# Kernel optimization log

Measured on AMD Instinct MI355X. Metric: run time of the kernel, lower is better.

## Reference

```python
import jax, jax.numpy as jnp
import numpy as np

B = 4096      # batch
D = 64        # state_dim
H = 512       # hidden_dim


def setup_inputs() -> dict:
    key = jax.random.key(0)
    ks = jax.random.split(key, 16)

    def init(k, shape, fan_in):
        return jax.random.normal(k, shape, dtype=jnp.float32) / np.float32(np.sqrt(fan_in))

    mu = jax.random.normal(ks[0], (B, D), dtype=jnp.float32)
    sigma_diag = 0.1 * jax.random.uniform(ks[1], (B, D), dtype=jnp.float32) + 0.01
    states = jnp.concatenate([mu, sigma_diag], axis=1)  # [B, 2D]

    return {
        "t": jnp.float32(0.5),
        "states": states,
        # dynamics net: tanh MLP D -> H -> H -> D
        "W1": init(ks[2], (H, D), D), "b1": jnp.zeros((H,), jnp.float32),
        "W2": init(ks[3], (H, H), H), "b2": jnp.zeros((H,), jnp.float32),
        "W3": init(ks[4], (D, H), H), "b3": jnp.zeros((D,), jnp.float32),
        # process-noise net: tanh MLP D -> H -> H -> D, softplus head (diagonal Q)
        "V1": init(ks[5], (H, D), D), "c1": jnp.zeros((H,), jnp.float32),
        "V2": init(ks[6], (H, H), H), "c2": jnp.zeros((H,), jnp.float32),
        "V3": init(ks[7], (D, H), H), "c3": jnp.zeros((D,), jnp.float32),
    }


def reference(t, states, W1, b1, W2, b2, W3, b3, V1, c1, V2, c2, V3, c3):
    # UPN ODE function, diagonal-covariance path.
    mu = states[:, :D]          # [B, D]
    sigma_diag = states[:, D:]  # [B, D]

    # dynamics MLP forward (t is an autonomous-system placeholder, unused)
    h1 = jnp.tanh(mu @ W1.T + b1)   # [B, H]
    h2 = jnp.tanh(h1 @ W2.T + b2)   # [B, H]
    mu_drift = h2 @ W3.T + b3       # [B, D]

    # analytic batched Jacobian of the tanh MLP: J = W3 diag(1-h2^2) W2 diag(1-h1^2) W1
    d1 = 1.0 - h1 * h1              # [B, H]
    d2 = 1.0 - h2 * h2              # [B, H]
    inner = jnp.einsum('hk,bk,kd->bhd', W2, d1, W1)   # [B, H, D]
    J = jnp.einsum('oh,bh,bhd->bod', W3, d2, inner)   # [B, D, D]
    J_diag = jnp.diagonal(J, axis1=1, axis2=2)        # [B, D]

    # process-noise net: diagonal Q, softplus ensures positivity
    g1 = jnp.tanh(mu @ V1.T + c1)
    g2 = jnp.tanh(g1 @ V2.T + c2)
    Q_diag = jax.nn.softplus(g2 @ V3.T + c3)          # [B, D]

    sigma_drift = 2.0 * J_diag * sigma_diag + Q_diag  # [B, D]
    return jnp.concatenate([mu_drift, sigma_drift], axis=1)  # [B, 2D]
```

## Files before the change

### kernel.cpp

```cpp
#include <hip/hip_runtime.h>
#include <hip/hip_bf16.h>

#define BB 4096
#define DD 64
#define HH 512

typedef __hip_bfloat16 bf16;
typedef _Float16 f16;
typedef __attribute__((ext_vector_type(8))) short bf16x8;
typedef __attribute__((ext_vector_type(8))) _Float16 f16x8;
typedef __attribute__((ext_vector_type(4))) float f32x4;

__device__ __forceinline__ float bf2f(bf16 x) { return __bfloat162float(x); }
__device__ __forceinline__ float u16tof(unsigned short u) {
  union { unsigned int i; float f; } v; v.i = ((unsigned int)u) << 16; return v.f;
}
#define BC8(p) __builtin_bit_cast(bf16x8, *(const uint4*)(p))
#define BCH8(p) __builtin_bit_cast(f16x8, *(const uint4*)(p))

__device__ __forceinline__ void gl16(const void* g, void* l) {
  __builtin_amdgcn_global_load_lds((__attribute__((address_space(1))) void*)g,
                                   (__attribute__((address_space(3))) void*)l,
                                   16, 0, 0);
}


__global__ __launch_bounds__(256) void cvt_weights(
    const float* __restrict__ W2, const float* __restrict__ V2,
    const float* __restrict__ W1, const float* __restrict__ V1,
    const float* __restrict__ W3, const float* __restrict__ V3,
    bf16* __restrict__ W2bf, bf16* __restrict__ V2bf,
    bf16* __restrict__ W1bf, bf16* __restrict__ V1bf,
    bf16* __restrict__ W3bf, bf16* __restrict__ V3bf,
    f16* __restrict__ W2fr, f16* __restrict__ W1sw, float* __restrict__ W3T) {
  int blk = blockIdx.x, t = threadIdx.x;
  if (blk < 512) {
    const float* src = (blk < 256) ? W2 : V2;
    bf16* dst = (blk < 256) ? W2bf : V2bf;
    int i = ((blk & 255) * 256 + t) * 4;
    float4 v = *(const float4*)(src + i);
    bf16 o[4] = {__float2bfloat16(v.x), __float2bfloat16(v.y),
                 __float2bfloat16(v.z), __float2bfloat16(v.w)};
    *(uint2*)(dst + i) = *(uint2*)o;
  } else if (blk < 640) {
    int uid = (blk - 512) * 256 + t;
    int col = (uid >> 2) & 511;
    int kc2s = uid >> 11;
    int kc = kc2s >> 1, s = kc2s & 1, q = uid & 3;
    const float* src = W2 + (size_t)col * HH + kc * 64 + s * 32 + q * 8;
    float4 a = *(const float4*)src;
    float4 b = *(const float4*)(src + 4);
    f16 o[8] = {(f16)a.x, (f16)a.y, (f16)a.z, (f16)a.w,
                (f16)b.x, (f16)b.y, (f16)b.z, (f16)b.w};
    *(uint4*)(W2fr + (size_t)uid * 8) = *(uint4*)o;
  } else if (blk < 656) {
    int uid = (blk - 640) * 256 + t;
    int kc = uid >> 9, rem = uid & 511;
    int dl = rem >> 3, u = rem & 7;
    f16 o[8];
#pragma unroll
    for (int e = 0; e < 8; ++e)
      o[e] = (f16)W1[(size_t)(kc * 64 + u * 8 + e) * DD + dl];
    *(uint4*)(W1sw + (size_t)((kc * 64 + dl) * 8 + (u ^ (dl & 7))) * 8) = *(uint4*)o;
  } else if (blk < 784) {
    int which = (blk - 656) >> 5;
    int local = (blk - 656) & 31;
    const float* src = (which == 0) ? W1 : (which == 1) ? V1 : (which == 2) ? W3 : V3;
    bf16* dst = (which == 0) ? W1bf : (which == 1) ? V1bf : (which == 2) ? W3bf : V3bf;
    int i = (local * 256 + t) * 4;
    float4 v = *(const float4*)(src + i);
    bf16 o[4] = {__float2bfloat16(v.x), __float2bfloat16(v.y),
                 __float2bfloat16(v.z), __float2bfloat16(v.w)};
    *(uint2*)(dst + i) = *(uint2*)o;
  } else {
    int e = ((blk - 784) * 256 + t) * 4;
    int h = e >> 6, o0 = e & 63;
    float o[4];
#pragma unroll
    for (int j = 0; j < 4; ++j) o[j] = W3[(size_t)(o0 + j) * HH + h];
    *(float4*)(W3T + (size_t)h * 64 + o0) = *(float4*)o;
  }
}

__global__ __launch_bounds__(256) void fwd(
    const float* __restrict__ states,
    const bf16* __restrict__ W1bf, const float* __restrict__ b1,
    const bf16* __restrict__ W2bf, const float* __restrict__ b2,
    const bf16* __restrict__ W3bf, const float* __restrict__ b3,
    const bf16* __restrict__ V1bf, const float* __restrict__ c1,
    const bf16* __restrict__ V2bf, const float* __restrict__ c2,
    const bf16* __restrict__ V3bf, const float* __restrict__ c3,
    bf16* __restrict__ Xbf, bf16* __restrict__ Ybf, float* __restrict__ out) {
  __shared__ __align__(16) bf16 mus[32 * 72];
  __shared__ __align__(16) bf16 Xres[32 * 520];
  __shared__ __align__(16) bf16 Bs[128 * 72];
  __shared__ __align__(16) bf16 Ych[32 * 136];
  const int bt = blockIdx.x * 32;
  const int path = blockIdx.y;
  const bf16* Wa = path ? V1bf : W1bf;
  const float* ba = path ? c1 : b1;
  const bf16* Wb = path ? V2bf : W2bf;
  const float* bbv = path ? c2 : b2;
  const bf16* Wc = path ? V3bf : W3bf;
  const float* bcv = path ? c3 : b3;
  const int t = threadIdx.x;
  const int lane = t & 63;
  const int w = t >> 6;
  const int c = lane & 15, q = lane >> 4;

  {
    int row = t >> 3, cg = (t & 7) * 8;
    bf16 o[8];
#pragma unroll
    for (int j = 0; j < 8; j += 4) {
      float4 v = *(const float4*)(states + (size_t)(bt + row) * 128 + cg + j);
      o[j] = __float2bfloat16(v.x); o[j + 1] = __float2bfloat16(v.y);
      o[j + 2] = __float2bfloat16(v.z); o[j + 3] = __float2bfloat16(v.w);
    }
    *(uint4*)(mus + row * 72 + cg) = *(const uint4*)o;
  }
  __syncthreads();

  for (int nch = 0; nch < 4; ++nch) {
    if (nch) __syncthreads();
#pragma unroll
    for (int i = 0; i < 4; ++i) {
      int g = t + i * 256;
      int row = g >> 3, kb = (g & 7) * 8;
      *(uint4*)(Bs + row * 72 + kb) =
          *(const uint4*)(Wa + (size_t)(nch * 128 + row) * 64 + kb);
    }
    __syncthreads();
    f32x4 acc1[2][2] = {};
#pragma unroll
    for (int s = 0; s < 2; ++s) {
      bf16x8 af0 = BC8(mus + c * 72 + s * 32 + q * 8);
      bf16x8 af1 = BC8(mus + (16 + c) * 72 + s * 32 + q * 8);
#pragma unroll
      for (int nt = 0; nt < 2; ++nt) {
        bf16x8 bfr = BC8(Bs + (w * 32 + nt * 16 + c) * 72 + s * 32 + q * 8);
        acc1[0][nt] = __builtin_amdgcn_mfma_f32_16x16x32_bf16(af0, bfr, acc1[0][nt], 0, 0, 0);
        acc1[1][nt] = __builtin_amdgcn_mfma_f32_16x16x32_bf16(af1, bfr, acc1[1][nt], 0, 0, 0);
      }
    }
#pragma unroll
    for (int nt = 0; nt < 2; ++nt) {
      int col = nch * 128 + w * 32 + nt * 16 + c;
      float bias = ba[col];
#pragma unroll
      for (int rb = 0; rb < 2; ++rb)
#pragma unroll
        for (int r = 0; r < 4; ++r) {
          int row = rb * 16 + q * 4 + r;
          float x = tanhf(acc1[rb][nt][r] + bias);
          Xres[row * 520 + col] = __float2bfloat16(x);
          if (!path) Xbf[(size_t)(bt + row) * HH + col] = __float2bfloat16(x);
        }
    }
  }
  __syncthreads();

  f32x4 acc3[2] = {};
  for (int hch = 0; hch < 4; ++hch) {
    f32x4 acc2[2][2] = {};
    for (int kc = 0; kc < 8; ++kc) {
      __syncthreads();
#pragma unroll
      for (int i = 0; i < 4; ++i) {
        int g = t + i * 256;
        int row = g >> 3, kb = (g & 7) * 8;
        *(uint4*)(Bs + row * 72 + kb) =
            *(const uint4*)(Wb + (size_t)(hch * 128 + row) * HH + kc * 64 + kb);
      }
      __syncthreads();
#pragma unroll
      for (int s = 0; s < 2; ++s) {
        bf16x8 af0 = BC8(Xres + c * 520 + kc * 64 + s * 32 + q * 8);
        bf16x8 af1 = BC8(Xres + (16 + c) * 520 + kc * 64 + s * 32 + q * 8);
#pragma unroll
        for (int nt = 0; nt < 2; ++nt) {
          bf16x8 bfr = BC8(Bs + (w * 32 + nt * 16 + c) * 72 + s * 32 + q * 8);
          acc2[0][nt] = __builtin_amdgcn_mfma_f32_16x16x32_bf16(af0, bfr, acc2[0][nt], 0, 0, 0);
          acc2[1][nt] = __builtin_amdgcn_mfma_f32_16x16x32_bf16(af1, bfr, acc2[1][nt], 0, 0, 0);
        }
      }
    }
    __syncthreads();
#pragma unroll
    for (int nt = 0; nt < 2; ++nt) {
      int hl = w * 32 + nt * 16 + c;
      int h = hch * 128 + hl;
      float bias = bbv[h];
#pragma unroll
      for (int rb = 0; rb < 2; ++rb)
#pragma unroll
        for (int r = 0; r < 4; ++r) {
          int row = rb * 16 + q * 4 + r;
          float y = tanhf(acc2[rb][nt][r] + bias);
          Ych[row * 136 + hl] = __float2bfloat16(y);
          if (!path) Ybf[(size_t)(bt + row) * HH + h] = __float2bfloat16(y);
        }
    }
    __syncthreads();
#pragma unroll
    for (int s3 = 0; s3 < 4; ++s3) {
      bf16x8 bf3 = BC8(Wc + (size_t)(w * 16 + c) * HH + hch * 128 + s3 * 32 + q * 8);
      bf16x8 af30 = BC8(Ych + c * 136 + s3 * 32 + q * 8);
      bf16x8 af31 = BC8(Ych + (16 + c) * 136 + s3 * 32 + q * 8);
      acc3[0] = __builtin_amdgcn_mfma_f32_16x16x32_bf16(af30, bf3, acc3[0], 0, 0, 0);
      acc3[1] = __builtin_amdgcn_mfma_f32_16x16x32_bf16(af31, bf3, acc3[1], 0, 0, 0);
    }
  }
  {
    int o = w * 16 + c;
    float bias = bcv[o];
#pragma unroll
    for (int rb = 0; rb < 2; ++rb)
#pragma unroll
      for (int r = 0; r < 4; ++r) {
        int row = rb * 16 + q * 4 + r;
        float v = acc3[rb][r] + bias;
        if (path) {
          v = fmaxf(v, 0.0f) + log1pf(expf(-fabsf(v)));
          out[(size_t)(bt + row) * 128 + 64 + o] = v;
        } else {
          out[(size_t)(bt + row) * 128 + o] = v;
        }
      }
  }
}

#define LDSW1 0
#define LDSD1 65536
#define LDSD2 73728
#define LDSRED 77824

__global__ __launch_bounds__(512, 2) void k4_gemm(
    const bf16* __restrict__ Xbf, const bf16* __restrict__ Ybf,
    const f16* __restrict__ W1sw, const f16* __restrict__ W2fr,
    const float* __restrict__ W3T, float* __restrict__ Jpart) {
  __shared__ __align__(16) char lds[81920];
  const int bt = blockIdx.x;
  const int h0 = blockIdx.y * 256;
  const int t = threadIdx.x;
  const int lane = t & 63;
  const int w = t >> 6;
  const int c = lane & 15, q = lane >> 4;
  const int wr = w >> 2, wc = w & 3;
  const int b0 = bt * 4;

#pragma unroll
  for (int i = 0; i < 8; ++i)
    gl16((const char*)W1sw + (t + i * 512) * 16,
         (char*)lds + LDSW1 + (t + i * 512) * 16);
  {
    int e = t * 4, j = e >> 9, k = e & 511;
    ushort4 xv = *(const ushort4*)((const unsigned short*)Xbf +
                                   (size_t)(b0 + j) * HH + k);
    f16 o[4];
    float x;
    x = u16tof(xv.x); o[0] = (f16)(1.f - x * x);
    x = u16tof(xv.y); o[1] = (f16)(1.f - x * x);
    x = u16tof(xv.z); o[2] = (f16)(1.f - x * x);
    x = u16tof(xv.w); o[3] = (f16)(1.f - x * x);
    *(uint2*)(lds + LDSD1 + e * 2) = *(uint2*)o;
  }
  {
    int e = t * 2, j = e >> 8, n = e & 255;
    ushort2 yv = *(const ushort2*)((const unsigned short*)Ybf +
                                   (size_t)(b0 + j) * HH + h0 + n);
    float y0 = u16tof(yv.x), y1 = u16tof(yv.y);
    float2 d2v = {1.f - y0 * y0, 1.f - y1 * y1};
    *(float2*)(lds + LDSD2 + e * 4) = d2v;
  }
  __syncthreads();

  const int cj = c & 7;
  const int j16_0 = ((0 + q) ^ cj) * 16;
  const int j16_1 = ((4 + q) ^ cj) * 16;
  const int arow = c * 128;
  const char* d1b = (const char*)lds + LDSD1 + wr * 2048 + q * 16;

  const char* gB = (const char*)W2fr + (size_t)(h0 + wc * 64) * 64 +
                   (c * 64 + q * 16);
#define BLD(kc_, s_, nt_) \
  BCH8(gB + ((kc_) * 2 + (s_)) * 32768 + (nt_) * 1024)

  f16x8 bb0[2][4], bb1[2][4];
#pragma unroll
  for (int nt = 0; nt < 4; ++nt) bb0[0][nt] = BLD(0, 0, nt);
#pragma unroll
  for (int nt = 0; nt < 4; ++nt) bb1[0][nt] = BLD(0, 1, nt);

  f32x4 acc[8][4] = {};

#pragma unroll
  for (int kc = 0; kc < 8; ++kc) {
    const int cur = kc & 1, nxt = cur ^ 1;
    if (kc < 7) {
#pragma unroll
      for (int nt = 0; nt < 4; ++nt) bb0[nxt][nt] = BLD(kc + 1, 0, nt);
#pragma unroll
      for (int nt = 0; nt < 4; ++nt) bb1[nxt][nt] = BLD(kc + 1, 1, nt);
    }
    const char* Ab = (const char*)lds + LDSW1 + kc * 8192;
    f16x8 a0[4], a1[4];
#pragma unroll
    for (int i = 0; i < 4; ++i) a0[i] = BCH8(Ab + arow + i * 2048 + j16_0);
#pragma unroll
    for (int i = 0; i < 4; ++i) a1[i] = BCH8(Ab + arow + i * 2048 + j16_1);
    f16x8 d00 = BCH8(d1b + kc * 128);
    f16x8 d10 = BCH8(d1b + 1024 + kc * 128);
    f16x8 d01 = BCH8(d1b + 64 + kc * 128);
    f16x8 d11 = BCH8(d1b + 1024 + 64 + kc * 128);

    f16x8 av;
    __builtin_amdgcn_s_setprio(1);
#pragma unroll
    for (int mt = 0; mt < 4; ++mt) {
      av = a0[mt] * d00;
#pragma unroll
      for (int nt = 0; nt < 4; ++nt)
        acc[mt][nt] = __builtin_amdgcn_mfma_f32_16x16x32_f16(
            av, bb0[cur][nt], acc[mt][nt], 0, 0, 0);
    }
#pragma unroll
    for (int mt = 0; mt < 4; ++mt) {
      av = a0[mt] * d10;
#pragma unroll
      for (int nt = 0; nt < 4; ++nt)
        acc[mt + 4][nt] = __builtin_amdgcn_mfma_f32_16x16x32_f16(
            av, bb0[cur][nt], acc[mt + 4][nt], 0, 0, 0);
    }
#pragma unroll
    for (int mt = 0; mt < 4; ++mt) {
      av = a1[mt] * d01;
#pragma unroll
      for (int nt = 0; nt < 4; ++nt)
        acc[mt][nt] = __builtin_amdgcn_mfma_f32_16x16x32_f16(
            av, bb1[cur][nt], acc[mt][nt], 0, 0, 0);
    }
#pragma unroll
    for (int mt = 0; mt < 4; ++mt) {
      av = a1[mt] * d11;
#pragma unroll
      for (int nt = 0; nt < 4; ++nt)
        acc[mt + 4][nt] = __builtin_amdgcn_mfma_f32_16x16x32_f16(
            av, bb1[cur][nt], acc[mt + 4][nt], 0, 0, 0);
    }
    __builtin_amdgcn_s_setprio(0);
    __builtin_amdgcn_sched_barrier(0);
  }
  __syncthreads();

#pragma unroll
  for (int i = 0; i < 8; ++i) {
    int e = (t + i * 512) * 4;
    int col = e >> 6, dl0 = e & 63;
    float4 v = *(const float4*)(W3T + (size_t)(h0 + col) * 64 + dl0);
    *(float4*)(lds + (col * 72 + dl0) * 4) = v;
  }
  __syncthreads();

  float d2r[2][4];
#pragma unroll
  for (int bh = 0; bh < 2; ++bh)
#pragma unroll
    for (int nt = 0; nt < 4; ++nt)
      d2r[bh][nt] = *(const float*)(
          lds + LDSD2 + ((wr * 2 + bh) * 256 + wc * 64 + nt * 16 + c) * 4);

  float vsum[8][4] = {};
#pragma unroll
  for (int mt4 = 0; mt4 < 4; ++mt4)
#pragma unroll
    for (int nt = 0; nt < 4; ++nt) {
      f32x4 w3v = *(const f32x4*)(
          lds + ((wc * 64 + nt * 16 + c) * 72 + mt4 * 16 + q * 4) * 4);
#pragma unroll
      for (int bh = 0; bh < 2; ++bh) {
        const int mt = bh * 4 + mt4;
        float sc = d2r[bh][nt];
#pragma unroll
        for (int r = 0; r < 4; ++r)
          vsum[mt][r] += acc[mt][nt][r] * w3v[r] * sc;
      }
    }

#pragma unroll
  for (int mt = 0; mt < 8; ++mt)
#pragma unroll
    for (int r = 0; r < 4; ++r) {
      float v = vsum[mt][r];
      v += __shfl_xor(v, 1);
      v += __shfl_xor(v, 2);
      v += __shfl_xor(v, 4);
      v += __shfl_xor(v, 8);
      if (c == 0)
        *(float*)(lds + LDSRED +
                  (wc * 256 + wr * 128 + mt * 16 + q * 4 + r) * 4) = v;
    }
  __syncthreads();
  if (t < 256) {
    float J = *(const float*)(lds + LDSRED + t * 4) +
              *(const float*)(lds + LDSRED + (256 + t) * 4) +
              *(const float*)(lds + LDSRED + (512 + t) * 4) +
              *(const float*)(lds + LDSRED + (768 + t) * 4);
    Jpart[(size_t)blockIdx.y * (BB * 64) + (size_t)bt * 256 + t] = J;
  }
}

__global__ __launch_bounds__(256) void combine(
    const float* __restrict__ Jpart, const float* __restrict__ states,
    float* __restrict__ out) {
  int idx = blockIdx.x * 256 + threadIdx.x;
  int b = idx >> 6, d = idx & 63;
  const int plane = BB * 64;
  float J = Jpart[idx] + Jpart[plane + idx];
  float sig = states[(size_t)b * 128 + 64 + d];
  float qd = out[(size_t)b * 128 + 64 + d];
  out[(size_t)b * 128 + 64 + d] = 2.0f * J * sig + qd;
}

extern "C" void kernel_launch(void* const* d_in, const int* in_sizes, int n_in,
                              void* d_out, int out_size, void* d_ws, size_t ws_size,
                              hipStream_t stream) {
  const float* states = (const float*)d_in[1];
  const float* W1 = (const float*)d_in[2];
  const float* b1 = (const float*)d_in[3];
  const float* W2 = (const float*)d_in[4];
  const float* b2 = (const float*)d_in[5];
  const float* W3 = (const float*)d_in[6];
  const float* b3 = (const float*)d_in[7];
  const float* V1 = (const float*)d_in[8];
  const float* c1 = (const float*)d_in[9];
  const float* V2 = (const float*)d_in[10];
  const float* c2 = (const float*)d_in[11];
  const float* V3 = (const float*)d_in[12];
  const float* c3 = (const float*)d_in[13];
  float* out = (float*)d_out;

  bf16* Xbf = (bf16*)d_ws;
  bf16* Ybf = Xbf + (size_t)BB * HH;
  bf16* W2bf = Ybf + (size_t)BB * HH;
  bf16* V2bf = W2bf + (size_t)HH * HH;
  bf16* W1bf = V2bf + (size_t)HH * HH;
  bf16* V1bf = W1bf + (size_t)HH * DD;
  bf16* W3bf = V1bf + (size_t)HH * DD;
  bf16* V3bf = W3bf + (size_t)DD * HH;
  f16* W1sw = (f16*)(V3bf + (size_t)DD * HH);
  f16* W2fr = W1sw + (size_t)DD * HH;
  float* W3T = (float*)(W2fr + (size_t)HH * HH);
  float* Jpart = W3T + (size_t)HH * DD;

  cvt_weights<<<dim3(816), 256, 0, stream>>>(W2, V2, W1, V1, W3, V3,
                                             W2bf, V2bf, W1bf, V1bf,
                                             W3bf, V3bf, W2fr, W1sw, W3T);
  fwd<<<dim3(128, 2), 256, 0, stream>>>(states, W1bf, b1, W2bf, b2, W3bf, b3,
                                        V1bf, c1, V2bf, c2, V3bf, c3,
                                        Xbf, Ybf, out);
  k4_gemm<<<dim3(1024, 2), 512, 0, stream>>>(Xbf, Ybf, W1sw, W2fr, W3T, Jpart);
  combine<<<dim3(1024), 256, 0, stream>>>(Jpart, states, out);
}
```

Before: 275.9 us.

## Make Jacobian kernel persistent over batch tiles and fuse combine step

The Jacobian GEMM kernel becomes a persistent grid of 256 blocks, each looping over four batch tiles and both hidden halves. The swizzled W1 tile is loaded into LDS once per block instead of once per tile, and the separate combine kernel and Jpart buffer are removed by accumulating the two halves in LDS and writing the sigma drift directly. W3T is now read from global memory instead of being staged in LDS, and the s_setprio hints are dropped. The risks are lower parallelism with 256 blocks of 512 threads, and a possible LDS race: the next tile writes new d1/d2 values before any barrier separates it from the previous tile's final reads.

```diff
diff --git a/kernel.cpp b/kernel.cpp
--- a/kernel.cpp
+++ b/kernel.cpp
@@ -234,192 +234,183 @@
 #define LDSD1 65536
 #define LDSD2 73728
 #define LDSRED 77824
+#define LDSJ 81920
 
 __global__ __launch_bounds__(512, 2) void k4_gemm(
     const bf16* __restrict__ Xbf, const bf16* __restrict__ Ybf,
     const f16* __restrict__ W1sw, const f16* __restrict__ W2fr,
-    const float* __restrict__ W3T, float* __restrict__ Jpart) {
-  __shared__ __align__(16) char lds[81920];
-  const int bt = blockIdx.x;
-  const int h0 = blockIdx.y * 256;
+    const float* __restrict__ W3T, const float* __restrict__ states,
+    float* __restrict__ out) {
+  __shared__ __align__(16) char lds[82944];
+  const int cu = blockIdx.x;
   const int t = threadIdx.x;
   const int lane = t & 63;
   const int w = t >> 6;
   const int c = lane & 15, q = lane >> 4;
   const int wr = w >> 2, wc = w & 3;
-  const int b0 = bt * 4;
-
-#pragma unroll
-  for (int i = 0; i < 8; ++i)
-    gl16((const char*)W1sw + (t + i * 512) * 16,
-         (char*)lds + LDSW1 + (t + i * 512) * 16);
-  {
-    int e = t * 4, j = e >> 9, k = e & 511;
-    ushort4 xv = *(const ushort4*)((const unsigned short*)Xbf +
-                                   (size_t)(b0 + j) * HH + k);
-    f16 o[4];
-    float x;
-    x = u16tof(xv.x); o[0] = (f16)(1.f - x * x);
-    x = u16tof(xv.y); o[1] = (f16)(1.f - x * x);
-    x = u16tof(xv.z); o[2] = (f16)(1.f - x * x);
-    x = u16tof(xv.w); o[3] = (f16)(1.f - x * x);
-    *(uint2*)(lds + LDSD1 + e * 2) = *(uint2*)o;
-  }
-  {
-    int e = t * 2, j = e >> 8, n = e & 255;
-    ushort2 yv = *(const ushort2*)((const unsigned short*)Ybf +
-                                   (size_t)(b0 + j) * HH + h0 + n);
-    float y0 = u16tof(yv.x), y1 = u16tof(yv.y);
-    float2 d2v = {1.f - y0 * y0, 1.f - y1 * y1};
-    *(float2*)(lds + LDSD2 + e * 4) = d2v;
-  }
-  __syncthreads();
-
   const int cj = c & 7;
   const int j16_0 = ((0 + q) ^ cj) * 16;
   const int j16_1 = ((4 + q) ^ cj) * 16;
   const int arow = c * 128;
   const char* d1b = (const char*)lds + LDSD1 + wr * 2048 + q * 16;
 
-  const char* gB = (const char*)W2fr + (size_t)(h0 + wc * 64) * 64 +
-                   (c * 64 + q * 16);
+#pragma unroll
+  for (int i = 0; i < 8; ++i)
+    gl16((const char*)W1sw + (t + i * 512) * 16,
+         (char*)lds + LDSW1 + (t + i * 512) * 16);
+
+#pragma unroll 1
+  for (int jt = 0; jt < 8; ++jt) {
+    const int bt = cu + (jt >> 1) * 256;
+    const int y = jt & 1;
+    const int h0 = y * 256;
+    const int b0 = bt * 4;
+
+    if (y == 0) {
+      int e = t * 4, j = e >> 9, k = e & 511;
+      ushort4 xv = *(const ushort4*)((const unsigned short*)Xbf +
+                                     (size_t)(b0 + j) * HH + k);
+      f16 o[4];
+      float x;
+      x = u16tof(xv.x); o[0] = (f16)(1.f - x * x);
+      x = u16tof(xv.y); o[1] = (f16)(1.f - x * x);
+      x = u16tof(xv.z); o[2] = (f16)(1.f - x * x);
+      x = u16tof(xv.w); o[3] = (f16)(1.f - x * x);
+      *(uint2*)(lds + LDSD1 + e * 2) = *(uint2*)o;
+    }
+    {
+      int e = t * 2, j = e >> 8, n = e & 255;
+      ushort2 yv = *(const ushort2*)((const unsigned short*)Ybf +
+                                     (size_t)(b0 + j) * HH + h0 + n);
+      float y0 = u16tof(yv.x), y1 = u16tof(yv.y);
+      float2 d2v = {1.f - y0 * y0, 1.f - y1 * y1};
+      *(float2*)(lds + LDSD2 + e * 4) = d2v;
+    }
+    __syncthreads();
+
+    const char* gB = (const char*)W2fr + (size_t)(h0 + wc * 64) * 64 +
+                     (c * 64 + q * 16);
 #define BLD(kc_, s_, nt_) \
   BCH8(gB + ((kc_) * 2 + (s_)) * 32768 + (nt_) * 1024)
 
-  f16x8 bb0[2][4], bb1[2][4];
-#pragma unroll
-  for (int nt = 0; nt < 4; ++nt) bb0[0][nt] = BLD(0, 0, nt);
-#pragma unroll
-  for (int nt = 0; nt < 4; ++nt) bb1[0][nt] = BLD(0, 1, nt);
-
-  f32x4 acc[8][4] = {};
-
-#pragma unroll
-  for (int kc = 0; kc < 8; ++kc) {
-    const int cur = kc & 1, nxt = cur ^ 1;
-    if (kc < 7) {
-#pragma unroll
-      for (int nt = 0; nt < 4; ++nt) bb0[nxt][nt] = BLD(kc + 1, 0, nt);
-#pragma unroll
-      for (int nt = 0; nt < 4; ++nt) bb1[nxt][nt] = BLD(kc + 1, 1, nt);
-    }
-    const char* Ab = (const char*)lds + LDSW1 + kc * 8192;
-    f16x8 a0[4], a1[4];
-#pragma unroll
-    for (int i = 0; i < 4; ++i) a0[i] = BCH8(Ab + arow + i * 2048 + j16_0);
-#pragma unroll
-    for (int i = 0; i < 4; ++i) a1[i] = BCH8(Ab + arow + i * 2048 + j16_1);
-    f16x8 d00 = BCH8(d1b + kc * 128);
-    f16x8 d10 = BCH8(d1b + 1024 + kc * 128);
-    f16x8 d01 = BCH8(d1b + 64 + kc * 128);
-    f16x8 d11 = BCH8(d1b + 1024 + 64 + kc * 128);
-
-    f16x8 av;
-    __builtin_amdgcn_s_setprio(1);
-#pragma unroll
-    for (int mt = 0; mt < 4; ++mt) {
-      av = a0[mt] * d00;
+    f16x8 bb0[2][4], bb1[2][4];
+#pragma unroll
+    for (int nt = 0; nt < 4; ++nt) bb0[0][nt] = BLD(0, 0, nt);
+#pragma unroll
+    for (int nt = 0; nt < 4; ++nt) bb1[0][nt] = BLD(0, 1, nt);
+
+    f32x4 acc[8][4] = {};
+
+#pragma unroll
+    for (int kc = 0; kc < 8; ++kc) {
+      const int cur = kc & 1, nxt = cur ^ 1;
+      if (kc < 7) {
+#pragma unroll
+        for (int nt = 0; nt < 4; ++nt) bb0[nxt][nt] = BLD(kc + 1, 0, nt);
+#pragma unroll
+        for (int nt = 0; nt < 4; ++nt) bb1[nxt][nt] = BLD(kc + 1, 1, nt);
+      }
+      const char* Ab = (const char*)lds + LDSW1 + kc * 8192;
+      f16x8 a0[4], a1[4];
+#pragma unroll
+      for (int i = 0; i < 4; ++i) a0[i] = BCH8(Ab + arow + i * 2048 + j16_0);
+#pragma unroll
+      for (int i = 0; i < 4; ++i) a1[i] = BCH8(Ab + arow + i * 2048 + j16_1);
+      f16x8 d00 = BCH8(d1b + kc * 128);
+      f16x8 d10 = BCH8(d1b + 1024 + kc * 128);
+      f16x8 d01 = BCH8(d1b + 64 + kc * 128);
+      f16x8 d11 = BCH8(d1b + 1024 + 64 + kc * 128);
+
+      f16x8 av;
+#pragma unroll
+      for (int mt = 0; mt < 4; ++mt) {
+        av = a0[mt] * d00;
+#pragma unroll
+        for (int nt = 0; nt < 4; ++nt)
+          acc[mt][nt] = __builtin_amdgcn_mfma_f32_16x16x32_f16(
+              av, bb0[cur][nt], acc[mt][nt], 0, 0, 0);
+      }
+#pragma unroll
+      for (int mt = 0; mt < 4; ++mt) {
+        av = a0[mt] * d10;
+#pragma unroll
+        for (int nt = 0; nt < 4; ++nt)
+          acc[mt + 4][nt] = __builtin_amdgcn_mfma_f32_16x16x32_f16(
+              av, bb0[cur][nt], acc[mt + 4][nt], 0, 0, 0);
+      }
+#pragma unroll
+      for (int mt = 0; mt < 4; ++mt) {
+        av = a1[mt] * d01;
+#pragma unroll
+        for (int nt = 0; nt < 4; ++nt)
+          acc[mt][nt] = __builtin_amdgcn_mfma_f32_16x16x32_f16(
+              av, bb1[cur][nt], acc[mt][nt], 0, 0, 0);
+      }
+#pragma unroll
+      for (int mt = 0; mt < 4; ++mt) {
+        av = a1[mt] * d11;
+#pragma unroll
+        for (int nt = 0; nt < 4; ++nt)
+          acc[mt + 4][nt] = __builtin_amdgcn_mfma_f32_16x16x32_f16(
+              av, bb1[cur][nt], acc[mt + 4][nt], 0, 0, 0);
+      }
+      __builtin_amdgcn_sched_barrier(0);
+    }
+
+    float d2r[2][4];
+#pragma unroll
+    for (int bh = 0; bh < 2; ++bh)
 #pragma unroll
       for (int nt = 0; nt < 4; ++nt)
-        acc[mt][nt] = __builtin_amdgcn_mfma_f32_16x16x32_f16(
-            av, bb0[cur][nt], acc[mt][nt], 0, 0, 0);
-    }
-#pragma unroll
-    for (int mt = 0; mt < 4; ++mt) {
-      av = a0[mt] * d10;
-#pragma unroll
-      for (int nt = 0; nt < 4; ++nt)
-        acc[mt + 4][nt] = __builtin_amdgcn_mfma_f32_16x16x32_f16(
-            av, bb0[cur][nt], acc[mt + 4][nt], 0, 0, 0);
-    }
-#pragma unroll
-    for (int mt = 0; mt < 4; ++mt) {
-      av = a1[mt] * d01;
-#pragma unroll
-      for (int nt = 0; nt < 4; ++nt)
-        acc[mt][nt] = __builtin_amdgcn_mfma_f32_16x16x32_f16(
-            av, bb1[cur][nt], acc[mt][nt], 0, 0, 0);
-    }
-#pragma unroll
-    for (int mt = 0; mt < 4; ++mt) {
-      av = a1[mt] * d11;
-#pragma unroll
-      for (int nt = 0; nt < 4; ++nt)
-        acc[mt + 4][nt] = __builtin_amdgcn_mfma_f32_16x16x32_f16(
-            av, bb1[cur][nt], acc[mt + 4][nt], 0, 0, 0);
-    }
-    __builtin_amdgcn_s_setprio(0);
-    __builtin_amdgcn_sched_barrier(0);
-  }
-  __syncthreads();
-
-#pragma unroll
-  for (int i = 0; i < 8; ++i) {
-    int e = (t + i * 512) * 4;
-    int col = e >> 6, dl0 = e & 63;
-    float4 v = *(const float4*)(W3T + (size_t)(h0 + col) * 64 + dl0);
-    *(float4*)(lds + (col * 72 + dl0) * 4) = v;
-  }
-  __syncthreads();
-
-  float d2r[2][4];
-#pragma unroll
-  for (int bh = 0; bh < 2; ++bh)
-#pragma unroll
-    for (int nt = 0; nt < 4; ++nt)
-      d2r[bh][nt] = *(const float*)(
-          lds + LDSD2 + ((wr * 2 + bh) * 256 + wc * 64 + nt * 16 + c) * 4);
-
-  float vsum[8][4] = {};
-#pragma unroll
-  for (int mt4 = 0; mt4 < 4; ++mt4)
-#pragma unroll
-    for (int nt = 0; nt < 4; ++nt) {
-      f32x4 w3v = *(const f32x4*)(
-          lds + ((wc * 64 + nt * 16 + c) * 72 + mt4 * 16 + q * 4) * 4);
-#pragma unroll
-      for (int bh = 0; bh < 2; ++bh) {
-        const int mt = bh * 4 + mt4;
-        float sc = d2r[bh][nt];
-#pragma unroll
-        for (int r = 0; r < 4; ++r)
-          vsum[mt][r] += acc[mt][nt][r] * w3v[r] * sc;
-      }
-    }
-
-#pragma unroll
-  for (int mt = 0; mt < 8; ++mt)
-#pragma unroll
-    for (int r = 0; r < 4; ++r) {
-      float v = vsum[mt][r];
-      v += __shfl_xor(v, 1);
-      v += __shfl_xor(v, 2);
-      v += __shfl_xor(v, 4);
-      v += __shfl_xor(v, 8);
-      if (c == 0)
-        *(float*)(lds + LDSRED +
-                  (wc * 256 + wr * 128 + mt * 16 + q * 4 + r) * 4) = v;
-    }
-  __syncthreads();
-  if (t < 256) {
-    float J = *(const float*)(lds + LDSRED + t * 4) +
-              *(const float*)(lds + LDSRED + (256 + t) * 4) +
-              *(const float*)(lds + LDSRED + (512 + t) * 4) +
-              *(const float*)(lds + LDSRED + (768 + t) * 4);
-    Jpart[(size_t)blockIdx.y * (BB * 64) + (size_t)bt * 256 + t] = J;
-  }
-}
-
-__global__ __launch_bounds__(256) void combine(
-    const float* __restrict__ Jpart, const float* __restrict__ states,
-    float* __restrict__ out) {
-  int idx = blockIdx.x * 256 + threadIdx.x;
-  int b = idx >> 6, d = idx & 63;
-  const int plane = BB * 64;
-  float J = Jpart[idx] + Jpart[plane + idx];
-  float sig = states[(size_t)b * 128 + 64 + d];
-  float qd = out[(size_t)b * 128 + 64 + d];
-  out[(size_t)b * 128 + 64 + d] = 2.0f * J * sig + qd;
+        d2r[bh][nt] = *(const float*)(
+            lds + LDSD2 + ((wr * 2 + bh) * 256 + wc * 64 + nt * 16 + c) * 4);
+
+    float vsum[8][4] = {};
+#pragma unroll
+    for (int mt4 = 0; mt4 < 4; ++mt4)
+#pragma unroll
+      for (int nt = 0; nt < 4; ++nt) {
+        f32x4 w3v = *(const f32x4*)(
+            W3T + (size_t)(h0 + wc * 64 + nt * 16 + c) * 64 + mt4 * 16 + q * 4);
+#pragma unroll
+        for (int bh = 0; bh < 2; ++bh) {
+          const int mt = bh * 4 + mt4;
+          float sc = d2r[bh][nt];
+#pragma unroll
+          for (int r = 0; r < 4; ++r)
+            vsum[mt][r] += acc[mt][nt][r] * w3v[r] * sc;
+        }
+      }
+
+#pragma unroll
+    for (int mt = 0; mt < 8; ++mt)
+#pragma unroll
+      for (int r = 0; r < 4; ++r) {
+        float v = vsum[mt][r];
+        v += __shfl_xor(v, 1);
+        v += __shfl_xor(v, 2);
+        v += __shfl_xor(v, 4);
+        v += __shfl_xor(v, 8);
+        if (c == 0)
+          *(float*)(lds + LDSRED +
+                    (wc * 256 + wr * 128 + mt * 16 + q * 4 + r) * 4) = v;
+      }
+    __syncthreads();
+    if (t < 256) {
+      float J = *(const float*)(lds + LDSRED + t * 4) +
+                *(const float*)(lds + LDSRED + (256 + t) * 4) +
+                *(const float*)(lds + LDSRED + (512 + t) * 4) +
+                *(const float*)(lds + LDSRED + (768 + t) * 4);
+      if (y == 0) {
+        *(float*)(lds + LDSJ + t * 4) = J;
+      } else {
+        J += *(const float*)(lds + LDSJ + t * 4);
+        size_t oi = (size_t)(b0 + (t >> 6)) * 128 + 64 + (t & 63);
+        float sig = states[oi];
+        out[oi] = 2.0f * J * sig + out[oi];
+      }
+    }
+  }
 }
 
 extern "C" void kernel_launch(void* const* d_in, const int* in_sizes, int n_in,
@@ -451,7 +442,6 @@
   f16* W1sw = (f16*)(V3bf + (size_t)DD * HH);
   f16* W2fr = W1sw + (size_t)DD * HH;
   float* W3T = (float*)(W2fr + (size_t)HH * HH);
-  float* Jpart = W3T + (size_t)HH * DD;
 
   cvt_weights<<<dim3(816), 256, 0, stream>>>(W2, V2, W1, V1, W3, V3,
                                              W2bf, V2bf, W1bf, V1bf,
@@ -459,6 +449,6 @@
   fwd<<<dim3(128, 2), 256, 0, stream>>>(states, W1bf, b1, W2bf, b2, W3bf, b3,
                                         V1bf, c1, V2bf, c2, V3bf, c3,
                                         Xbf, Ybf, out);
-  k4_gemm<<<dim3(1024, 2), 512, 0, stream>>>(Xbf, Ybf, W1sw, W2fr, W3T, Jpart);
-  combine<<<dim3(1024), 256, 0, stream>>>(Jpart, states, out);
-}
+  k4_gemm<<<dim3(256), 512, 0, stream>>>(Xbf, Ybf, W1sw, W2fr, W3T,
+                                         states, out);
+}
```

Measured after the change: 298.1 us. +8.0%, slower.
